# Optimization experiments

Hardware: AMD Instinct MI355X
Metric: run time of the kernel (lower is better)

## Reference

```python
import jax, jax.numpy as jnp
import numpy as np

D = 512
N_WAY = 64
K_SHOT = 16
N_QUERY = 8192


def setup_inputs() -> dict:
    key = jax.random.key(0)
    k1, k2, k3, k4 = jax.random.split(key, 4)
    support = jax.random.normal(k1, (N_WAY * K_SHOT, D), dtype=jnp.float32)
    query = jax.random.normal(k2, (N_QUERY, D), dtype=jnp.float32)
    # nn.Linear(input_dim, input_dim) params (kaiming-uniform-ish scale)
    bound = 1.0 / np.sqrt(D)
    W = jax.random.uniform(k3, (D, D), minval=-bound, maxval=bound, dtype=jnp.float32)
    b = jax.random.uniform(k4, (D,), minval=-bound, maxval=bound, dtype=jnp.float32)
    return {"support": support, "query": query, "W": W, "b": b,
            "n_way": N_WAY, "k_shot": K_SHOT}


def reference(support, query, W, b, n_way, k_shot):
    # shared linear projection: x @ W^T + b (torch nn.Linear convention)
    support_emb = support @ W.T + b            # [n_way*k_shot, d]
    query_emb = query @ W.T + b                # [n_q, d]
    # class prototypes: mean over the k_shot axis
    prototypes = support_emb.reshape(n_way, k_shot, -1).mean(axis=1)  # [n_way, d]
    # pairwise squared euclidean distances (broadcast sub/square/sum,
    # same math as the torch euclidean_dist)
    diff = query_emb[:, None, :] - prototypes[None, :, :]  # [n_q, n_way, d]
    dists = jnp.sum(diff * diff, axis=-1)                  # [n_q, n_way]
    return dists
```

## Files before the change

kernel.cpp:

```cpp
#include <hip/hip_runtime.h>
#include <hip/hip_bf16.h>

#define D 512
#define NWAY 64
#define KSHOT 16
#define NQ 8192

typedef __bf16 bf16_t;
typedef __bf16 bf16x8_t __attribute__((ext_vector_type(8)));
typedef __bf16 bf16x4_t __attribute__((ext_vector_type(4)));
typedef float  f32x4    __attribute__((ext_vector_type(4)));

typedef __attribute__((address_space(1))) const void gv_t;
typedef __attribute__((address_space(3))) void lv_t;
__device__ __forceinline__ void ld16(const void* g, void* l) {
    __builtin_amdgcn_global_load_lds((gv_t*)g, (lv_t*)l, 16, 0, 0);
}


__global__ __launch_bounds__(256) void k_prep(
    const float* __restrict__ sup, const float* __restrict__ W,
    const float* __restrict__ bias, bf16_t* __restrict__ Bsw,
    bf16_t* __restrict__ Psw)
{
    const int b = blockIdx.x, t = threadIdx.x;

    if (b < 256) {
        const int c = b >> 2, jq = b & 3;
        __shared__ __align__(16) float cm[D];
        {
            const int d = t * 2;
            float sx = 0.f, sy = 0.f;
#pragma unroll
            for (int j = 0; j < KSHOT; ++j) {
                float2 v = *(const float2*)(sup + (size_t)(c * KSHOT + j) * D + d);
                sx += v.x; sy += v.y;
            }
            cm[d] = sx * (1.0f / KSHOT); cm[d + 1] = sy * (1.0f / KSHOT);
        }
        __syncthreads();
        const int j = jq * 128 + (t >> 1);
        const int half = t & 1;
        const f32x4* wr = (const f32x4*)(W + (size_t)j * D + half * 256);
        const f32x4* cr = (const f32x4*)(cm + half * 256);
        float s = 0.f;
#pragma unroll 8
        for (int i = 0; i < 64; ++i) {
            f32x4 a = cr[i], wv = wr[i];
            s += a[0]*wv[0] + a[1]*wv[1] + a[2]*wv[2] + a[3]*wv[3];
        }
        s += __shfl_xor(s, 1);
        if (!half) {
            const float v = s + bias[j];
            const int sP = j >> 3;
            const int pos = (sP & ~7) | ((sP & 7) ^ (c & 7));
            Psw[c * 512 + pos * 8 + (j & 7)] = (bf16_t)v;
        }
        return;
    }

    {
        const int n = (b - 256) * 4 + (t >> 6);
        const int sl = t & 63;
        const f32x4* wp = (const f32x4*)(W + (size_t)n * D + sl * 8);
        f32x4 v0 = wp[0], v1 = wp[1];
        bf16x8_t hv = { (bf16_t)v0[0], (bf16_t)v0[1], (bf16_t)v0[2], (bf16_t)v0[3],
                        (bf16_t)v1[0], (bf16_t)v1[1], (bf16_t)v1[2], (bf16_t)v1[3] };
        const int ck = sl >> 3, s = sl & 7;
        *(bf16x8_t*)(Bsw + (size_t)ck * 32768 + n * 64 + ((s ^ (n & 7)) * 8)) = hv;
    }
}

__global__ __launch_bounds__(512, 2) void k_main(
    const float* __restrict__ query, const bf16_t* __restrict__ Bsw,
    const bf16_t* __restrict__ Psw, const float* __restrict__ bias,
    float* __restrict__ out)
{
    __shared__ __align__(16) bf16_t Bb[2][32768];
    __shared__ __align__(16) bf16_t Ab[2][2048];
    __shared__ float qln[4][32];
    __shared__ float phs[NWAY];
    __shared__ float bs[512];

    const int t = threadIdx.x, bm = blockIdx.x;
    bs[t] = bias[t];

    const int l = t & 63, w = t >> 6;
    const int wm = w & 1, wn = w >> 1;
    const int r15 = l & 15, quad = l >> 4;

    const int xt0 = ((quad ^ (r15 & 7)) * 8);
    const int xt1 = (((4 + quad) ^ (r15 & 7)) * 8);
    const int aoff = (wm * 16 + r15) * 64;
    const int boff = (wn * 128 + r15) * 64;

    const int am = t >> 4;
    const int ac4 = t & 15;
    const int a_lds = am * 64 + (((ac4 >> 1) ^ (am & 7)) * 8) + (ac4 & 1) * 4;
    const float* aqp = query + (size_t)(bm * 32 + am) * D + ac4 * 4;

    bf16x4_t areg[8];
#pragma unroll
    for (int ck = 0; ck < 8; ++ck) {
        f32x4 v = *(const f32x4*)(aqp + ck * 64);
        areg[ck] = (bf16x4_t){ (bf16_t)v[0], (bf16_t)v[1], (bf16_t)v[2], (bf16_t)v[3] };
    }

    f32x4 acc[8];
#pragma unroll
    for (int i = 0; i < 8; ++i) acc[i] = (f32x4){0.f, 0.f, 0.f, 0.f};

    {
#pragma unroll
        for (int i = 0; i < 8; ++i) {
            const int off = t * 8 + i * 4096;
            ld16(Bsw + off, &Bb[0][off]);
        }
        *(bf16x4_t*)(&Ab[0][a_lds]) = areg[0];
    }
    __syncthreads();

#pragma unroll
    for (int ck = 0; ck < 8; ++ck) {
        const int cur = ck & 1;
        if (ck < 7) {
            const int nxt = cur ^ 1;
            const size_t sb = (size_t)(ck + 1) * 32768;
#pragma unroll
            for (int i = 0; i < 8; ++i) {
                const int off = t * 8 + i * 4096;
                ld16(Bsw + sb + off, &Bb[nxt][off]);
            }
            *(bf16x4_t*)(&Ab[nxt][a_lds]) = areg[ck + 1];
        } else {
#pragma unroll
            for (int i = 0; i < 8; ++i) {
                const int off = t * 8 + i * 4096;
                ld16(Psw + off, &Bb[0][off]);
            }
        }

        bf16x8_t a0 = *(const bf16x8_t*)(&Ab[cur][aoff + xt0]);
        bf16x8_t a1 = *(const bf16x8_t*)(&Ab[cur][aoff + xt1]);
#pragma unroll
        for (int tt = 0; tt < 8; ++tt) {
            bf16x8_t b0 = *(const bf16x8_t*)(&Bb[cur][boff + tt * 1024 + xt0]);
            bf16x8_t b1 = *(const bf16x8_t*)(&Bb[cur][boff + tt * 1024 + xt1]);
            acc[tt] = __builtin_amdgcn_mfma_f32_16x16x32_bf16(a0, b0, acc[tt], 0, 0, 0);
            acc[tt] = __builtin_amdgcn_mfma_f32_16x16x32_bf16(a1, b1, acc[tt], 0, 0, 0);
        }

        if (ck < 7) __syncthreads();
    }
    __syncthreads();

    bf16_t* Ex = &Bb[1][0];
    float qp[4] = {0.f, 0.f, 0.f, 0.f};
#pragma unroll
    for (int tt = 0; tt < 8; ++tt) {
        const int k = wn * 128 + tt * 16 + r15;
        const int s = k >> 3, klo = k & 7;
        const float bv = bs[k];
#pragma unroll
        for (int reg = 0; reg < 4; ++reg) {
            const int row = wm * 16 + quad * 4 + reg;
            const float v = acc[tt][reg] + bv;
            qp[reg] += v * v;
            const int pos = (s & ~7) | ((s & 7) ^ (row & 7));
            Ex[row * 512 + pos * 8 + klo] = (bf16_t)v;
        }
    }
#pragma unroll
    for (int reg = 0; reg < 4; ++reg) {
        float s = qp[reg];
        s += __shfl_xor(s, 1); s += __shfl_xor(s, 2);
        s += __shfl_xor(s, 4); s += __shfl_xor(s, 8);
        if (r15 == 0) qln[wn][wm * 16 + quad * 4 + reg] = s;
    }

    if (t < NWAY) {
        const bf16_t* pr = &Bb[0][t * 512];
        float s2 = 0.f;
#pragma unroll
        for (int i = 0; i < 64; ++i) {
            bf16x8_t v = *(const bf16x8_t*)(pr + i * 8);
#pragma unroll
            for (int e = 0; e < 8; ++e) { float f = (float)v[e]; s2 += f * f; }
        }
        phs[t] = s2;
    }
    __syncthreads();

    f32x4 cacc[4];
#pragma unroll
    for (int ct = 0; ct < 4; ++ct) cacc[ct] = (f32x4){0.f, 0.f, 0.f, 0.f};
    const bf16_t* Pl = &Bb[0][0];
#pragma unroll
    for (int kk = 0; kk < 4; ++kk) {
        const int s = wn * 16 + kk * 4 + quad;
        const int pos = (s & ~7) | ((s & 7) ^ (r15 & 7));
        bf16x8_t af = *(const bf16x8_t*)(Ex + (wm * 16 + r15) * 512 + pos * 8);
#pragma unroll
        for (int ct = 0; ct < 4; ++ct) {
            bf16x8_t bf = *(const bf16x8_t*)(Pl + (ct * 16 + r15) * 512 + pos * 8);
            cacc[ct] = __builtin_amdgcn_mfma_f32_16x16x32_bf16(af, bf, cacc[ct], 0, 0, 0);
        }
    }

    f32x4* ex = (f32x4*)&Bb[1][16384];
#pragma unroll
    for (int ct = 0; ct < 4; ++ct)
        ex[((wm * 4 + ct) * 4 + wn) * 64 + l] = cacc[ct];
    __syncthreads();

    f32x4 cf = ex[((wm * 4 + wn) * 4 + 0) * 64 + l];
#pragma unroll
    for (int wnp = 1; wnp < 4; ++wnp)
        cf = cf + ex[((wm * 4 + wn) * 4 + wnp) * 64 + l];

#pragma unroll
    for (int reg = 0; reg < 4; ++reg) {
        const int row_local = wm * 16 + quad * 4 + reg;
        const float qt = qln[0][row_local] + qln[1][row_local] +
                         qln[2][row_local] + qln[3][row_local];
        const int rowg = bm * 32 + row_local;
        const int c = wn * 16 + r15;
        out[(size_t)rowg * NWAY + c] = qt + phs[c] - 2.0f * cf[reg];
    }
}

extern "C" void kernel_launch(void* const* d_in, const int* in_sizes, int n_in,
                              void* d_out, int out_size, void* d_ws, size_t ws_size,
                              hipStream_t stream)
{
    const float* support = (const float*)d_in[0];
    const float* query   = (const float*)d_in[1];
    const float* W       = (const float*)d_in[2];
    const float* bias    = (const float*)d_in[3];
    float* out = (float*)d_out;

    char* ws = (char*)d_ws;
    bf16_t* Bsw = (bf16_t*)ws;
    bf16_t* Psw = (bf16_t*)(ws + 524288);

    k_prep<<<384, 256, 0, stream>>>(support, W, bias, Bsw, Psw);
    k_main<<<256, 512, 0, stream>>>(query, Bsw, Psw, bias, out);
}
```

Before: 99.39 us.

## Double query rows per block to halve W reloads and restructure distance epilogue

Each block now handles 64 query rows instead of 32, so each wave computes two 16-row MFMA tiles that share the same B (W) fragments. The number of blocks drops from 256 to 128, which halves total global/LDS traffic for the projection weight per output. The epilogue distance GEMM is reorganized so each wave covers a 16-row by 32-class tile over the full K, removing the cross-wave LDS reduction and one barrier. With only 128 blocks the grid no longer fills all 256 CUs, and register pressure rises from the doubled accumulators.

New measurement: 101.9 us. +2.6%, slower.

```diff
diff --git a/kernel.cpp b/kernel.cpp
--- a/kernel.cpp
+++ b/kernel.cpp
@@ -5,6 +5,7 @@
 #define NWAY 64
 #define KSHOT 16
 #define NQ 8192
+#define BM 64
 
 typedef __bf16 bf16_t;
 typedef __bf16 bf16x8_t __attribute__((ext_vector_type(8)));
@@ -77,8 +78,8 @@
     float* __restrict__ out)
 {
     __shared__ __align__(16) bf16_t Bb[2][32768];
-    __shared__ __align__(16) bf16_t Ab[2][2048];
-    __shared__ float qln[4][32];
+    __shared__ __align__(16) bf16_t Ab[2][4096];
+    __shared__ float qln[4][BM];
     __shared__ float phs[NWAY];
     __shared__ float bs[512];
 
@@ -91,24 +92,29 @@
 
     const int xt0 = ((quad ^ (r15 & 7)) * 8);
     const int xt1 = (((4 + quad) ^ (r15 & 7)) * 8);
-    const int aoff = (wm * 16 + r15) * 64;
+    const int aoff0 = (wm * 32 + r15) * 64;
+    const int aoff1 = (wm * 32 + 16 + r15) * 64;
     const int boff = (wn * 128 + r15) * 64;
 
-    const int am = t >> 4;
-    const int ac4 = t & 15;
-    const int a_lds = am * 64 + (((ac4 >> 1) ^ (am & 7)) * 8) + (ac4 & 1) * 4;
-    const float* aqp = query + (size_t)(bm * 32 + am) * D + ac4 * 4;
-
-    bf16x4_t areg[8];
+    const int am = t >> 3;
+    const int as = t & 7;
+    const int a_lds = am * 64 + ((as ^ (am & 7)) * 8);
+    const float* aqp = query + (size_t)(bm * BM + am) * D + as * 8;
+
+    bf16x8_t areg[8];
 #pragma unroll
     for (int ck = 0; ck < 8; ++ck) {
-        f32x4 v = *(const f32x4*)(aqp + ck * 64);
-        areg[ck] = (bf16x4_t){ (bf16_t)v[0], (bf16_t)v[1], (bf16_t)v[2], (bf16_t)v[3] };
-    }
-
-    f32x4 acc[8];
-#pragma unroll
-    for (int i = 0; i < 8; ++i) acc[i] = (f32x4){0.f, 0.f, 0.f, 0.f};
+        f32x4 v0 = *(const f32x4*)(aqp + ck * 64);
+        f32x4 v1 = *(const f32x4*)(aqp + ck * 64 + 4);
+        areg[ck] = (bf16x8_t){ (bf16_t)v0[0], (bf16_t)v0[1], (bf16_t)v0[2], (bf16_t)v0[3],
+                               (bf16_t)v1[0], (bf16_t)v1[1], (bf16_t)v1[2], (bf16_t)v1[3] };
+    }
+
+    f32x4 acc[2][8];
+#pragma unroll
+    for (int rt = 0; rt < 2; ++rt)
+#pragma unroll
+        for (int i = 0; i < 8; ++i) acc[rt][i] = (f32x4){0.f, 0.f, 0.f, 0.f};
 
     {
 #pragma unroll
@@ -116,7 +122,7 @@
             const int off = t * 8 + i * 4096;
             ld16(Bsw + off, &Bb[0][off]);
         }
-        *(bf16x4_t*)(&Ab[0][a_lds]) = areg[0];
+        *(bf16x8_t*)(&Ab[0][a_lds]) = areg[0];
     }
     __syncthreads();
 
@@ -131,7 +137,7 @@
                 const int off = t * 8 + i * 4096;
                 ld16(Bsw + sb + off, &Bb[nxt][off]);
             }
-            *(bf16x4_t*)(&Ab[nxt][a_lds]) = areg[ck + 1];
+            *(bf16x8_t*)(&Ab[nxt][a_lds]) = areg[ck + 1];
         } else {
 #pragma unroll
             for (int i = 0; i < 8; ++i) {
@@ -140,14 +146,18 @@
             }
         }
 
-        bf16x8_t a0 = *(const bf16x8_t*)(&Ab[cur][aoff + xt0]);
-        bf16x8_t a1 = *(const bf16x8_t*)(&Ab[cur][aoff + xt1]);
+        bf16x8_t a00 = *(const bf16x8_t*)(&Ab[cur][aoff0 + xt0]);
+        bf16x8_t a01 = *(const bf16x8_t*)(&Ab[cur][aoff0 + xt1]);
+        bf16x8_t a10 = *(const bf16x8_t*)(&Ab[cur][aoff1 + xt0]);
+        bf16x8_t a11 = *(const bf16x8_t*)(&Ab[cur][aoff1 + xt1]);
 #pragma unroll
         for (int tt = 0; tt < 8; ++tt) {
             bf16x8_t b0 = *(const bf16x8_t*)(&Bb[cur][boff + tt * 1024 + xt0]);
             bf16x8_t b1 = *(const bf16x8_t*)(&Bb[cur][boff + tt * 1024 + xt1]);
-            acc[tt] = __builtin_amdgcn_mfma_f32_16x16x32_bf16(a0, b0, acc[tt], 0, 0, 0);
-            acc[tt] = __builtin_amdgcn_mfma_f32_16x16x32_bf16(a1, b1, acc[tt], 0, 0, 0);
+            acc[0][tt] = __builtin_amdgcn_mfma_f32_16x16x32_bf16(a00, b0, acc[0][tt], 0, 0, 0);
+            acc[0][tt] = __builtin_amdgcn_mfma_f32_16x16x32_bf16(a01, b1, acc[0][tt], 0, 0, 0);
+            acc[1][tt] = __builtin_amdgcn_mfma_f32_16x16x32_bf16(a10, b0, acc[1][tt], 0, 0, 0);
+            acc[1][tt] = __builtin_amdgcn_mfma_f32_16x16x32_bf16(a11, b1, acc[1][tt], 0, 0, 0);
         }
 
         if (ck < 7) __syncthreads();
@@ -155,27 +165,31 @@
     __syncthreads();
 
     bf16_t* Ex = &Bb[1][0];
-    float qp[4] = {0.f, 0.f, 0.f, 0.f};
+    float qp[2][4] = {{0.f,0.f,0.f,0.f},{0.f,0.f,0.f,0.f}};
 #pragma unroll
     for (int tt = 0; tt < 8; ++tt) {
         const int k = wn * 128 + tt * 16 + r15;
         const int s = k >> 3, klo = k & 7;
         const float bv = bs[k];
 #pragma unroll
+        for (int rt = 0; rt < 2; ++rt)
+#pragma unroll
         for (int reg = 0; reg < 4; ++reg) {
-            const int row = wm * 16 + quad * 4 + reg;
-            const float v = acc[tt][reg] + bv;
-            qp[reg] += v * v;
+            const int row = wm * 32 + rt * 16 + quad * 4 + reg;
+            const float v = acc[rt][tt][reg] + bv;
+            qp[rt][reg] += v * v;
             const int pos = (s & ~7) | ((s & 7) ^ (row & 7));
             Ex[row * 512 + pos * 8 + klo] = (bf16_t)v;
         }
     }
 #pragma unroll
+    for (int rt = 0; rt < 2; ++rt)
+#pragma unroll
     for (int reg = 0; reg < 4; ++reg) {
-        float s = qp[reg];
+        float s = qp[rt][reg];
         s += __shfl_xor(s, 1); s += __shfl_xor(s, 2);
         s += __shfl_xor(s, 4); s += __shfl_xor(s, 8);
-        if (r15 == 0) qln[wn][wm * 16 + quad * 4 + reg] = s;
+        if (r15 == 0) qln[wn][wm * 32 + rt * 16 + quad * 4 + reg] = s;
     }
 
     if (t < NWAY) {
@@ -191,41 +205,34 @@
     }
     __syncthreads();
 
-    f32x4 cacc[4];
-#pragma unroll
-    for (int ct = 0; ct < 4; ++ct) cacc[ct] = (f32x4){0.f, 0.f, 0.f, 0.f};
+    const int ert = w >> 1, ecg = w & 1;
+    f32x4 cacc[2];
+    cacc[0] = (f32x4){0.f, 0.f, 0.f, 0.f};
+    cacc[1] = (f32x4){0.f, 0.f, 0.f, 0.f};
     const bf16_t* Pl = &Bb[0][0];
 #pragma unroll
-    for (int kk = 0; kk < 4; ++kk) {
-        const int s = wn * 16 + kk * 4 + quad;
-        const int pos = (s & ~7) | ((s & 7) ^ (r15 & 7));
-        bf16x8_t af = *(const bf16x8_t*)(Ex + (wm * 16 + r15) * 512 + pos * 8);
-#pragma unroll
-        for (int ct = 0; ct < 4; ++ct) {
-            bf16x8_t bf = *(const bf16x8_t*)(Pl + (ct * 16 + r15) * 512 + pos * 8);
-            cacc[ct] = __builtin_amdgcn_mfma_f32_16x16x32_bf16(af, bf, cacc[ct], 0, 0, 0);
-        }
-    }
-
-    f32x4* ex = (f32x4*)&Bb[1][16384];
-#pragma unroll
-    for (int ct = 0; ct < 4; ++ct)
-        ex[((wm * 4 + ct) * 4 + wn) * 64 + l] = cacc[ct];
-    __syncthreads();
-
-    f32x4 cf = ex[((wm * 4 + wn) * 4 + 0) * 64 + l];
-#pragma unroll
-    for (int wnp = 1; wnp < 4; ++wnp)
-        cf = cf + ex[((wm * 4 + wn) * 4 + wnp) * 64 + l];
+    for (int kk = 0; kk < 16; ++kk) {
+        const int s = kk * 4 + quad;
+        const int posA = (s & ~7) | ((s & 7) ^ (r15 & 7));
+        bf16x8_t af = *(const bf16x8_t*)(Ex + (ert * 16 + r15) * 512 + posA * 8);
+#pragma unroll
+        for (int j = 0; j < 2; ++j) {
+            bf16x8_t bf = *(const bf16x8_t*)(Pl + ((ecg * 2 + j) * 16 + r15) * 512 + posA * 8);
+            cacc[j] = __builtin_amdgcn_mfma_f32_16x16x32_bf16(af, bf, cacc[j], 0, 0, 0);
+        }
+    }
 
 #pragma unroll
     for (int reg = 0; reg < 4; ++reg) {
-        const int row_local = wm * 16 + quad * 4 + reg;
+        const int row_local = ert * 16 + quad * 4 + reg;
         const float qt = qln[0][row_local] + qln[1][row_local] +
                          qln[2][row_local] + qln[3][row_local];
-        const int rowg = bm * 32 + row_local;
-        const int c = wn * 16 + r15;
-        out[(size_t)rowg * NWAY + c] = qt + phs[c] - 2.0f * cf[reg];
+        const int rowg = bm * BM + row_local;
+#pragma unroll
+        for (int j = 0; j < 2; ++j) {
+            const int c = (ecg * 2 + j) * 16 + r15;
+            out[(size_t)rowg * NWAY + c] = qt + phs[c] - 2.0f * cacc[j][reg];
+        }
     }
 }
 
@@ -244,5 +251,5 @@
     bf16_t* Psw = (bf16_t*)(ws + 524288);
 
     k_prep<<<384, 256, 0, stream>>>(support, W, bias, Bsw, Psw);
-    k_main<<<256, 512, 0, stream>>>(query, Bsw, Psw, bias, out);
-}
+    k_main<<<128, 512, 0, stream>>>(query, Bsw, Psw, bias, out);
+}
```
